# Optimization experiments

Measured on AMD Instinct MI355X. Metric: run time of the kernel, lower is better.

Reference implementation:

```python
import jax, jax.numpy as jnp
import numpy as np

B, LQ, LK, D = 32, 2048, 2048, 64


def setup_inputs() -> dict:
    key = jax.random.key(0)
    k1, k2, k3, k4 = jax.random.split(key, 4)
    querys = jax.random.normal(k1, (B, LQ, D), dtype=jnp.float32)
    keys = jax.random.normal(k2, (B, LK, D), dtype=jnp.float32)
    values = jax.random.normal(k3, (B, LK, D), dtype=jnp.float32)
    # valid lengths in [1, LK]
    valid_lens = jax.random.randint(k4, (B,), 1, LK + 1, dtype=jnp.int32)
    return {"querys": querys, "keys": keys, "values": values, "valid_lens": valid_lens}


def reference(querys, keys, values, valid_lens):
    d = querys.shape[-1]
    # [B, Lq, Lk] score matrix
    scores = jnp.einsum("bqd,bkd->bqk", querys, keys) / jnp.sqrt(jnp.asarray(d, querys.dtype))
    # masked softmax: key positions >= valid_len get -1e6 (as in d2l masked_softmax)
    key_pos = jnp.arange(scores.shape[-1], dtype=jnp.int32)  # [Lk]
    mask = key_pos[None, None, :] < valid_lens[:, None, None]  # [B, 1, Lk]
    scores = jnp.where(mask, scores, jnp.asarray(-1e6, scores.dtype))
    attn = jax.nn.softmax(scores, axis=-1)
    # dropout p=0.0 -> identity
    return jnp.einsum("bqk,bkd->bqd", attn, values)
```

## Files before the change

### kernel.cpp

```cpp
#include <hip/hip_runtime.h>
#include <hip/hip_bf16.h>
#include <math.h>


#define B_    32
#define LQ_   2048
#define LK_   2048
#define D_    64

typedef __attribute__((ext_vector_type(8)))  short bf16x8;
typedef __attribute__((ext_vector_type(4)))  float f32x4;
typedef __attribute__((ext_vector_type(16))) float f32x16;
typedef __attribute__((ext_vector_type(2)))  unsigned u32x2;

static __device__ __forceinline__ unsigned pk_bf16(float a, float b) {
    __hip_bfloat162 h = __float22bfloat162_rn(float2{a, b});
    return *(unsigned*)&h;
}

static __device__ __forceinline__ u32x2 plswap(unsigned a, unsigned b) {
    return __builtin_amdgcn_permlane32_swap(a, b, false, false);
}
static __device__ __forceinline__ float xhalf_max(float x) {
    u32x2 r = plswap(__float_as_uint(x), __float_as_uint(x));
    return fmaxf(__uint_as_float(r[0]), __uint_as_float(r[1]));
}
static __device__ __forceinline__ float xhalf_add(float x) {
    u32x2 r = plswap(__float_as_uint(x), __float_as_uint(x));
    return __uint_as_float(r[0]) + __uint_as_float(r[1]);
}

template<int NS>
__global__ __launch_bounds__(256, 6) void fa_split10_kernel(
    const float* __restrict__ Q, const float* __restrict__ K,
    const float* __restrict__ V, const int* __restrict__ vlen,
    float* __restrict__ OP, float* __restrict__ ML)
{
    __shared__ __align__(16) short Kl[2][64 * 64];
    __shared__ __align__(16) short Vt[2][64 * 64];

    const int tid  = threadIdx.x;
    const int wid  = tid >> 6;
    const int lane = tid & 63;
    const int c31  = lane & 31;
    const int h    = lane >> 5;

    constexpr int PB = 16 * NS;
    const int L    = blockIdx.x;
    const int rank = L / PB;
    const int sub  = L % PB;
    const int qb   = sub & 15;
    const int s    = sub >> 4;
    int b;
    {
        const int vj = vlen[c31];
        int r = 0;
#pragma unroll
        for (int k = 0; k < 32; ++k) {
            const int vk = __shfl(vj, k);
            r += (vk > vj) || (vk == vj && k < c31);
        }
        const unsigned long long match = __ballot(r == rank);
        b = (int)(__ffsll(match) - 1) & 31;
    }
    const int q0 = qb * 128 + wid * 32;
    const int vl = vlen[b];
    const int nt    = (vl + 63) >> 6;
    const int chunk = (nt + NS - 1) / NS;
    const int t0    = s * chunk;
    const int t1    = min(t0 + chunk, nt);

    const float qscale = 0.125f * 1.44269504088896340736f;

    unsigned qfrag[4][4];
#pragma unroll
    for (int ks = 0; ks < 4; ++ks) {
        const float* qp = Q + ((size_t)(b * LQ_ + q0 + c31)) * D_ + ks * 16 + h * 8;
        f32x4 t0v = *(const f32x4*)qp;
        f32x4 t1v = *(const f32x4*)(qp + 4);
#pragma unroll
        for (int jj = 0; jj < 2; ++jj) {
            qfrag[ks][jj]     = pk_bf16(t0v[2*jj] * qscale, t0v[2*jj+1] * qscale);
            qfrag[ks][jj + 2] = pk_bf16(t1v[2*jj] * qscale, t1v[2*jj+1] * qscale);
        }
    }

    f32x16 oacc[2];
#pragma unroll
    for (int dt = 0; dt < 2; ++dt)
#pragma unroll
        for (int r = 0; r < 16; ++r) oacc[dt][r] = 0.f;
    float mrun = -INFINITY, lrun = 0.f;

    const int skey = tid >> 2, skh = tid & 3;
    const int vkg = tid >> 4, vdg = tid & 15;

    const float* kgp = K + ((size_t)(b * LK_ + skey)) * D_ + skh * 16;
    const float* vgp = V + ((size_t)(b * LK_ + vkg * 4)) * D_ + vdg * 4;

    f32x4 kr[4], vr[4];
    if (t0 < t1) {
        const size_t off = (size_t)t0 * 64 * D_;
#pragma unroll
        for (int i = 0; i < 4; ++i) kr[i] = *(const f32x4*)(kgp + off + 4 * i);
#pragma unroll
        for (int i = 0; i < 4; ++i) vr[i] = *(const f32x4*)(vgp + off + (size_t)i * D_);
    }

    for (int t = t0; t < t1; ++t) {
        const int k0 = t * 64;
        const int buf = t & 1;

        {
            unsigned pk32[8];
#pragma unroll
            for (int m = 0; m < 8; ++m)
                pk32[m] = pk_bf16(kr[m >> 1][2 * (m & 1)], kr[m >> 1][2 * (m & 1) + 1]);
#pragma unroll
            for (int cch = 0; cch < 2; ++cch) {
                const int pos = (skh * 2 + cch) ^ (skey & 7);
                *(bf16x8*)&Kl[buf][skey * 64 + pos * 8] = *(bf16x8*)&pk32[4 * cch];
            }
#pragma unroll
            for (int dr = 0; dr < 4; ++dr) {
                const unsigned w0 = pk_bf16(vr[0][dr], vr[1][dr]);
                const unsigned w1 = pk_bf16(vr[2][dr], vr[3][dr]);
                const int dim = vdg * 4 + dr;
                const int pos = (vkg >> 1) ^ (dim & 7);
                uint2* dst = (uint2*)&Vt[buf][dim * 64 + pos * 8 + (vkg & 1) * 4];
                *dst = uint2{w0, w1};
            }
        }
        __syncthreads();

        if (t + 1 < t1) {
            const float* kn = kgp + (size_t)(k0 + 64) * D_;
            const float* vn = vgp + (size_t)(k0 + 64) * D_;
#pragma unroll
            for (int i = 0; i < 4; ++i) kr[i] = *(const f32x4*)(kn + 4 * i);
#pragma unroll
            for (int i = 0; i < 4; ++i) vr[i] = *(const f32x4*)(vn + (size_t)i * D_);
        }

        f32x16 st[2];
#pragma unroll
        for (int ss = 0; ss < 2; ++ss) {
#pragma unroll
            for (int r = 0; r < 16; ++r) st[ss][r] = 0.f;
#pragma unroll
            for (int ks = 0; ks < 4; ++ks) {
                const int pos = (ks * 2 + h) ^ (c31 & 7);
                bf16x8 kf = *(const bf16x8*)&Kl[buf][(ss * 32 + c31) * 64 + pos * 8];
                st[ss] = __builtin_amdgcn_mfma_f32_32x32x16_bf16(
                    kf, *(const bf16x8*)&qfrag[ks][0], st[ss], 0, 0, 0);
            }
        }

        if (k0 + 64 > vl) {
#pragma unroll
            for (int ss = 0; ss < 2; ++ss) {
                const int base = k0 + ss * 32 + 4 * h;
#pragma unroll
                for (int r = 0; r < 16; ++r) {
                    const int key = base + (r & 3) + 8 * (r >> 2);
                    if (key >= vl) st[ss][r] = -1e30f;
                }
            }
        }

        float m8[8];
#pragma unroll
        for (int r = 0; r < 8; ++r)
            m8[r] = fmaxf(fmaxf(st[0][r], st[0][r + 8]),
                          fmaxf(st[1][r], st[1][r + 8]));
#pragma unroll
        for (int o = 4; o; o >>= 1)
#pragma unroll
            for (int r = 0; r < o; ++r) m8[r] = fmaxf(m8[r], m8[r + o]);
        const float tm = xhalf_max(m8[0]);

        if (__any(tm > mrun + 8.f)) {
            const float mnew = fmaxf(mrun, tm);
            const float corr = exp2f(mrun - mnew);
            lrun *= corr;
#pragma unroll
            for (int dt = 0; dt < 2; ++dt)
#pragma unroll
                for (int r = 0; r < 16; ++r) oacc[dt][r] *= corr;
            mrun = mnew;
        }
#pragma unroll
        for (int ss = 0; ss < 2; ++ss)
#pragma unroll
            for (int r = 0; r < 16; ++r)
                st[ss][r] = exp2f(st[ss][r] - mrun);
        float s8[8];
#pragma unroll
        for (int r = 0; r < 8; ++r)
            s8[r] = (st[0][r] + st[0][r + 8]) + (st[1][r] + st[1][r + 8]);
#pragma unroll
        for (int o = 4; o; o >>= 1)
#pragma unroll
            for (int r = 0; r < o; ++r) s8[r] += s8[r + o];
        lrun += xhalf_add(s8[0]);

        unsigned pk[2][8];
#pragma unroll
        for (int ss = 0; ss < 2; ++ss)
#pragma unroll
            for (int m = 0; m < 8; ++m)
                pk[ss][m] = pk_bf16(st[ss][2 * m], st[ss][2 * m + 1]);

#pragma unroll
        for (int kq = 0; kq < 4; ++kq) {
            const int ss = kq >> 1, A4 = (kq & 1) * 4;
            u32x2 r02 = plswap(pk[ss][A4],     pk[ss][A4 + 2]);
            u32x2 r13 = plswap(pk[ss][A4 + 1], pk[ss][A4 + 3]);
            unsigned pf[4] = {r02[0], r13[0], r02[1], r13[1]};
            const bf16x8 pfr = *(const bf16x8*)&pf[0];
#pragma unroll
            for (int dt = 0; dt < 2; ++dt) {
                const int pos = (kq * 2 + h) ^ (c31 & 7);
                bf16x8 vf = *(const bf16x8*)&Vt[buf][(dt * 32 + c31) * 64 + pos * 8];
                oacc[dt] = __builtin_amdgcn_mfma_f32_32x32x16_bf16(vf, pfr, oacc[dt], 0, 0, 0);
            }
        }
    }

    const size_t row = (size_t)s * (B_ * LQ_) + b * LQ_ + q0 + c31;
    float* op = OP + row * D_;
#pragma unroll
    for (int dt = 0; dt < 2; ++dt)
#pragma unroll
        for (int g = 0; g < 4; ++g) {
            f32x4 v;
#pragma unroll
            for (int j = 0; j < 4; ++j) v[j] = oacc[dt][4 * g + j];
            *(f32x4*)(op + dt * 32 + 8 * g + 4 * h) = v;
        }
    if (h == 0)
        *(float2*)&ML[row * 2] = float2{mrun, lrun};
}

template<int NS>
__global__ __launch_bounds__(256) void fa_merge_kernel(
    const float* __restrict__ OP, const float* __restrict__ ML,
    float* __restrict__ O)
{
    const int g   = blockIdx.x * 256 + threadIdx.x;
    const int row = g >> 4;
    const int qd  = (g & 15) * 4;

    float mf = -INFINITY;
#pragma unroll
    for (int s = 0; s < NS; ++s) {
        float2 ml = *(const float2*)&ML[((size_t)s * (B_ * LQ_) + row) * 2];
        mf = fmaxf(mf, ml.x);
    }
    float den = 0.f;
    f32x4 acc = {0.f, 0.f, 0.f, 0.f};
#pragma unroll
    for (int s = 0; s < NS; ++s) {
        const size_t srow = (size_t)s * (B_ * LQ_) + row;
        float2 ml = *(const float2*)&ML[srow * 2];
        const float c = exp2f(ml.x - mf);
        den += c * ml.y;
        f32x4 v = *(const f32x4*)&OP[srow * D_ + qd];
        acc += v * c;
    }
    const float inv = 1.f / den;
    *(f32x4*)(O + (size_t)row * D_ + qd) = acc * inv;
}

__global__ __launch_bounds__(128, 2) void fa_mono_kernel(
    const float* __restrict__ Q, const float* __restrict__ K,
    const float* __restrict__ V, const int* __restrict__ vlen,
    float* __restrict__ O)
{
    __shared__ __align__(16) short Kl[2][64 * 64];
    __shared__ __align__(16) short Vt[2][64 * 64];

    const int tid  = threadIdx.x;
    const int wave = tid >> 6;
    const int lane = tid & 63;
    const int c31  = lane & 31;
    const int h    = lane >> 5;

    const int b  = blockIdx.y;
    const int q0 = blockIdx.x * 64 + wave * 32;
    const int vl = vlen[b];
    const int nt = (vl + 63) >> 6;

    const float qscale = 0.125f * 1.44269504088896340736f;

    unsigned qfrag[4][4];
#pragma unroll
    for (int ks = 0; ks < 4; ++ks) {
        const float* qp = Q + ((size_t)(b * LQ_ + q0 + c31)) * D_ + ks * 16 + h * 8;
        f32x4 t0 = *(const f32x4*)qp;
        f32x4 t1 = *(const f32x4*)(qp + 4);
#pragma unroll
        for (int jj = 0; jj < 2; ++jj) {
            qfrag[ks][jj]     = pk_bf16(t0[2*jj] * qscale, t0[2*jj+1] * qscale);
            qfrag[ks][jj + 2] = pk_bf16(t1[2*jj] * qscale, t1[2*jj+1] * qscale);
        }
    }

    f32x16 oacc[2];
#pragma unroll
    for (int dt = 0; dt < 2; ++dt)
#pragma unroll
        for (int r = 0; r < 16; ++r) oacc[dt][r] = 0.f;
    float mrun = -INFINITY, lrun = 0.f;

    const int skey = tid >> 1, skh = tid & 1;
    const int vkg = tid >> 4, vdg = tid & 15;

    const float* kgp = K + ((size_t)(b * LK_ + skey)) * D_ + skh * 32;
    const float* vgp = V + ((size_t)(b * LK_ + vkg * 8)) * D_ + vdg * 4;

    f32x4 kr[8], vr[8];
#pragma unroll
    for (int i = 0; i < 8; ++i) kr[i] = *(const f32x4*)(kgp + 4 * i);
#pragma unroll
    for (int i = 0; i < 8; ++i) vr[i] = *(const f32x4*)(vgp + (size_t)i * D_);

    for (int t = 0; t < nt; ++t) {
        const int k0 = t * 64;
        const int buf = t & 1;
        {
            unsigned pk32[16];
#pragma unroll
            for (int m = 0; m < 16; ++m)
                pk32[m] = pk_bf16(kr[m >> 1][2 * (m & 1)], kr[m >> 1][2 * (m & 1) + 1]);
#pragma unroll
            for (int cch = 0; cch < 4; ++cch) {
                const int pos = (skh * 4 + cch) ^ (skey & 7);
                *(bf16x8*)&Kl[buf][skey * 64 + pos * 8] = *(bf16x8*)&pk32[4 * cch];
            }
#pragma unroll
            for (int dr = 0; dr < 4; ++dr) {
                unsigned w[4];
#pragma unroll
                for (int p = 0; p < 4; ++p)
                    w[p] = pk_bf16(vr[2 * p][dr], vr[2 * p + 1][dr]);
                const int dim = vdg * 4 + dr;
                const int pos = vkg ^ (dim & 7);
                *(bf16x8*)&Vt[buf][dim * 64 + pos * 8] = *(bf16x8*)&w[0];
            }
        }
        if (t + 1 < nt) {
            const float* kn = kgp + (size_t)(k0 + 64) * D_;
            const float* vn = vgp + (size_t)(k0 + 64) * D_;
#pragma unroll
            for (int i = 0; i < 8; ++i) kr[i] = *(const f32x4*)(kn + 4 * i);
#pragma unroll
            for (int i = 0; i < 8; ++i) vr[i] = *(const f32x4*)(vn + (size_t)i * D_);
        }
        __syncthreads();

        f32x16 st[2];
#pragma unroll
        for (int ss = 0; ss < 2; ++ss) {
#pragma unroll
            for (int r = 0; r < 16; ++r) st[ss][r] = 0.f;
#pragma unroll
            for (int ks = 0; ks < 4; ++ks) {
                const int pos = (ks * 2 + h) ^ (c31 & 7);
                bf16x8 kf = *(const bf16x8*)&Kl[buf][(ss * 32 + c31) * 64 + pos * 8];
                st[ss] = __builtin_amdgcn_mfma_f32_32x32x16_bf16(
                    kf, *(const bf16x8*)&qfrag[ks][0], st[ss], 0, 0, 0);
            }
        }
        if (k0 + 64 > vl) {
#pragma unroll
            for (int ss = 0; ss < 2; ++ss) {
                const int base = k0 + ss * 32 + 4 * h;
#pragma unroll
                for (int r = 0; r < 16; ++r) {
                    const int key = base + (r & 3) + 8 * (r >> 2);
                    if (key >= vl) st[ss][r] = -1e30f;
                }
            }
        }
        float tm = st[0][0];
#pragma unroll
        for (int ss = 0; ss < 2; ++ss)
#pragma unroll
            for (int r = 0; r < 16; ++r) tm = fmaxf(tm, st[ss][r]);
        tm = fmaxf(tm, __shfl_xor(tm, 32));
        if (__any(tm > mrun + 8.f)) {
            const float mnew = fmaxf(mrun, tm);
            const float corr = exp2f(mrun - mnew);
            lrun *= corr;
#pragma unroll
            for (int dt = 0; dt < 2; ++dt)
#pragma unroll
                for (int r = 0; r < 16; ++r) oacc[dt][r] *= corr;
            mrun = mnew;
        }
        float rs = 0.f;
#pragma unroll
        for (int ss = 0; ss < 2; ++ss)
#pragma unroll
            for (int r = 0; r < 16; ++r) {
                const float p = exp2f(st[ss][r] - mrun);
                st[ss][r] = p;
                rs += p;
            }
        rs += __shfl_xor(rs, 32);
        lrun += rs;

        unsigned pk[2][8];
#pragma unroll
        for (int ss = 0; ss < 2; ++ss)
#pragma unroll
            for (int m = 0; m < 8; ++m)
                pk[ss][m] = pk_bf16(st[ss][2 * m], st[ss][2 * m + 1]);
#pragma unroll
        for (int kq = 0; kq < 4; ++kq) {
            const int ss = kq >> 1, A4 = (kq & 1) * 4;
            unsigned p0 = pk[ss][A4], p1 = pk[ss][A4+1], p2 = pk[ss][A4+2], p3 = pk[ss][A4+3];
            unsigned xp0 = __shfl_xor((int)p0, 32);
            unsigned xp1 = __shfl_xor((int)p1, 32);
            unsigned xp2 = __shfl_xor((int)p2, 32);
            unsigned xp3 = __shfl_xor((int)p3, 32);
            unsigned pf[4];
            pf[0] = h ? xp2 : p0;
            pf[1] = h ? xp3 : p1;
            pf[2] = h ? p2  : xp0;
            pf[3] = h ? p3  : xp1;
            const bf16x8 pfr = *(const bf16x8*)&pf[0];
#pragma unroll
            for (int dt = 0; dt < 2; ++dt) {
                const int pos = (kq * 2 + h) ^ (c31 & 7);
                bf16x8 vf = *(const bf16x8*)&Vt[buf][(dt * 32 + c31) * 64 + pos * 8];
                oacc[dt] = __builtin_amdgcn_mfma_f32_32x32x16_bf16(vf, pfr, oacc[dt], 0, 0, 0);
            }
        }
    }

    const float inv = 1.f / lrun;
    float* op = O + ((size_t)(b * LQ_ + q0 + c31)) * D_;
#pragma unroll
    for (int dt = 0; dt < 2; ++dt)
#pragma unroll
        for (int g = 0; g < 4; ++g) {
            f32x4 v;
#pragma unroll
            for (int j = 0; j < 4; ++j) v[j] = oacc[dt][4 * g + j] * inv;
            *(f32x4*)(op + dt * 32 + 8 * g + 4 * h) = v;
        }
}

extern "C" void kernel_launch(void* const* d_in, const int* in_sizes, int n_in,
                              void* d_out, int out_size, void* d_ws, size_t ws_size,
                              hipStream_t stream) {
    const float* Q    = (const float*)d_in[0];
    const float* K    = (const float*)d_in[1];
    const float* V    = (const float*)d_in[2];
    const int*   vlen = (const int*)d_in[3];
    float*       O    = (float*)d_out;

    const size_t rows = (size_t)B_ * LQ_;
    auto need = [&](int ns) { return (size_t)ns * rows * (D_ + 2) * sizeof(float); };

    int NS = 0;
    if      (d_ws && ws_size >= need(4)) NS = 4;
    else if (d_ws && ws_size >= need(2)) NS = 2;
    else if (d_ws && ws_size >= need(1)) NS = 1;

    if (NS == 0) {
        dim3 grid(LQ_ / 64, B_);
        fa_mono_kernel<<<grid, dim3(128), 0, stream>>>(Q, K, V, vlen, O);
        return;
    }

    float* OP = (float*)d_ws;
    float* ML = (float*)d_ws + (size_t)NS * rows * D_;

    const unsigned nblk = (unsigned)(16 * B_ * NS);
    switch (NS) {
        case 4: fa_split10_kernel<4><<<dim3(nblk), dim3(256), 0, stream>>>(Q, K, V, vlen, OP, ML); break;
        case 2: fa_split10_kernel<2><<<dim3(nblk), dim3(256), 0, stream>>>(Q, K, V, vlen, OP, ML); break;
        default: fa_split10_kernel<1><<<dim3(nblk), dim3(256), 0, stream>>>(Q, K, V, vlen, OP, ML); break;
    }

    dim3 g2((unsigned)((rows * (D_ / 4)) / 256));
    switch (NS) {
        case 4: fa_merge_kernel<4><<<g2, dim3(256), 0, stream>>>(OP, ML, O); break;
        case 2: fa_merge_kernel<2><<<g2, dim3(256), 0, stream>>>(OP, ML, O); break;
        default: fa_merge_kernel<1><<<g2, dim3(256), 0, stream>>>(OP, ML, O); break;
    }
}
```

Measured before the change: 161.4 us.

## Pre-convert K/V to bf16 (V transposed) and store split partials in bf16

```diff
diff --git a/kernel.cpp b/kernel.cpp
--- a/kernel.cpp
+++ b/kernel.cpp
@@ -17,6 +17,12 @@
     __hip_bfloat162 h = __float22bfloat162_rn(float2{a, b});
     return *(unsigned*)&h;
 }
+static __device__ __forceinline__ float bf_lo(unsigned u) {
+    return __uint_as_float(u << 16);
+}
+static __device__ __forceinline__ float bf_hi(unsigned u) {
+    return __uint_as_float(u & 0xffff0000u);
+}
 
 static __device__ __forceinline__ u32x2 plswap(unsigned a, unsigned b) {
     return __builtin_amdgcn_permlane32_swap(a, b, false, false);
@@ -30,11 +36,48 @@
     return __uint_as_float(r[0]) + __uint_as_float(r[1]);
 }
 
+__global__ __launch_bounds__(256) void fa_cvt_kernel(
+    const float* __restrict__ K, const float* __restrict__ V,
+    short* __restrict__ Kb, short* __restrict__ Vtb)
+{
+    const int tid = threadIdx.x;
+    const int b   = blockIdx.y;
+    const int k0  = blockIdx.x * 64;
+
+    {
+        const int kk = tid >> 2, q4 = tid & 3;
+        const size_t off = ((size_t)(b * LK_ + k0 + kk)) * D_ + q4 * 16;
+        const float* src = K + off;
+        unsigned w[8];
+#pragma unroll
+        for (int i = 0; i < 4; ++i) {
+            f32x4 v = *(const f32x4*)(src + 4 * i);
+            w[2 * i]     = pk_bf16(v[0], v[1]);
+            w[2 * i + 1] = pk_bf16(v[2], v[3]);
+        }
+        short* dst = Kb + off;
+        *(bf16x8*)dst       = *(bf16x8*)&w[0];
+        *(bf16x8*)(dst + 8) = *(bf16x8*)&w[4];
+    }
+    {
+        const int vkg = tid & 15, vdg = tid >> 4;
+        f32x4 vv[4];
+#pragma unroll
+        for (int p = 0; p < 4; ++p)
+            vv[p] = *(const f32x4*)&V[((size_t)(b * LK_ + k0 + vkg * 4 + p)) * D_ + vdg * 4];
+#pragma unroll
+        for (int dr = 0; dr < 4; ++dr) {
+            uint2 w = { pk_bf16(vv[0][dr], vv[1][dr]), pk_bf16(vv[2][dr], vv[3][dr]) };
+            *(uint2*)&Vtb[((size_t)(b * 64 + vdg * 4 + dr)) * LK_ + k0 + vkg * 4] = w;
+        }
+    }
+}
+
 template<int NS>
-__global__ __launch_bounds__(256, 6) void fa_split10_kernel(
-    const float* __restrict__ Q, const float* __restrict__ K,
-    const float* __restrict__ V, const int* __restrict__ vlen,
-    float* __restrict__ OP, float* __restrict__ ML)
+__global__ __launch_bounds__(256, 2) void fa_split12_kernel(
+    const float* __restrict__ Q, const short* __restrict__ Kb,
+    const short* __restrict__ Vtb, const int* __restrict__ vlen,
+    short* __restrict__ OP, float* __restrict__ ML)
 {
     __shared__ __align__(16) short Kl[2][64 * 64];
     __shared__ __align__(16) short Vt[2][64 * 64];
@@ -93,18 +136,19 @@
     float mrun = -INFINITY, lrun = 0.f;
 
     const int skey = tid >> 2, skh = tid & 3;
-    const int vkg = tid >> 4, vdg = tid & 15;
-
-    const float* kgp = K + ((size_t)(b * LK_ + skey)) * D_ + skh * 16;
-    const float* vgp = V + ((size_t)(b * LK_ + vkg * 4)) * D_ + vdg * 4;
-
-    f32x4 kr[4], vr[4];
+    const int vdim = skey, vkh = skh;
+
+    const short* kbp = Kb  + ((size_t)(b * LK_ + skey)) * D_ + skh * 16;
+    const short* vtp = Vtb + ((size_t)(b * 64 + vdim)) * LK_ + vkh * 16;
+
+    bf16x8 kr0, kr1, vr0, vr1;
     if (t0 < t1) {
-        const size_t off = (size_t)t0 * 64 * D_;
-#pragma unroll
-        for (int i = 0; i < 4; ++i) kr[i] = *(const f32x4*)(kgp + off + 4 * i);
-#pragma unroll
-        for (int i = 0; i < 4; ++i) vr[i] = *(const f32x4*)(vgp + off + (size_t)i * D_);
+        const short* kp = kbp + (size_t)t0 * 64 * D_;
+        const short* vp = vtp + (size_t)t0 * 64;
+        kr0 = *(const bf16x8*)(kp);
+        kr1 = *(const bf16x8*)(kp + 8);
+        vr0 = *(const bf16x8*)(vp);
+        vr1 = *(const bf16x8*)(vp + 8);
     }
 
     for (int t = t0; t < t1; ++t) {
@@ -112,34 +156,24 @@
         const int buf = t & 1;
 
         {
-            unsigned pk32[8];
-#pragma unroll
-            for (int m = 0; m < 8; ++m)
-                pk32[m] = pk_bf16(kr[m >> 1][2 * (m & 1)], kr[m >> 1][2 * (m & 1) + 1]);
-#pragma unroll
-            for (int cch = 0; cch < 2; ++cch) {
-                const int pos = (skh * 2 + cch) ^ (skey & 7);
-                *(bf16x8*)&Kl[buf][skey * 64 + pos * 8] = *(bf16x8*)&pk32[4 * cch];
-            }
-#pragma unroll
-            for (int dr = 0; dr < 4; ++dr) {
-                const unsigned w0 = pk_bf16(vr[0][dr], vr[1][dr]);
-                const unsigned w1 = pk_bf16(vr[2][dr], vr[3][dr]);
-                const int dim = vdg * 4 + dr;
-                const int pos = (vkg >> 1) ^ (dim & 7);
-                uint2* dst = (uint2*)&Vt[buf][dim * 64 + pos * 8 + (vkg & 1) * 4];
-                *dst = uint2{w0, w1};
-            }
+            const int pk0 = (skh * 2)     ^ (skey & 7);
+            const int pk1 = (skh * 2 + 1) ^ (skey & 7);
+            *(bf16x8*)&Kl[buf][skey * 64 + pk0 * 8] = kr0;
+            *(bf16x8*)&Kl[buf][skey * 64 + pk1 * 8] = kr1;
+            const int pv0 = (vkh * 2)     ^ (vdim & 7);
+            const int pv1 = (vkh * 2 + 1) ^ (vdim & 7);
+            *(bf16x8*)&Vt[buf][vdim * 64 + pv0 * 8] = vr0;
+            *(bf16x8*)&Vt[buf][vdim * 64 + pv1 * 8] = vr1;
         }
         __syncthreads();
 
         if (t + 1 < t1) {
-            const float* kn = kgp + (size_t)(k0 + 64) * D_;
-            const float* vn = vgp + (size_t)(k0 + 64) * D_;
-#pragma unroll
-            for (int i = 0; i < 4; ++i) kr[i] = *(const f32x4*)(kn + 4 * i);
-#pragma unroll
-            for (int i = 0; i < 4; ++i) vr[i] = *(const f32x4*)(vn + (size_t)i * D_);
+            const short* kp = kbp + (size_t)(k0 + 64) * D_;
+            const short* vp = vtp + (size_t)(k0 + 64);
+            kr0 = *(const bf16x8*)(kp);
+            kr1 = *(const bf16x8*)(kp + 8);
+            vr0 = *(const bf16x8*)(vp);
+            vr1 = *(const bf16x8*)(vp + 8);
         }
 
         f32x16 st[2];
@@ -228,15 +262,14 @@
     }
 
     const size_t row = (size_t)s * (B_ * LQ_) + b * LQ_ + q0 + c31;
-    float* op = OP + row * D_;
+    short* op = OP + row * D_;
 #pragma unroll
     for (int dt = 0; dt < 2; ++dt)
 #pragma unroll
         for (int g = 0; g < 4; ++g) {
-            f32x4 v;
-#pragma unroll
-            for (int j = 0; j < 4; ++j) v[j] = oacc[dt][4 * g + j];
-            *(f32x4*)(op + dt * 32 + 8 * g + 4 * h) = v;
+            const unsigned w0 = pk_bf16(oacc[dt][4 * g],     oacc[dt][4 * g + 1]);
+            const unsigned w1 = pk_bf16(oacc[dt][4 * g + 2], oacc[dt][4 * g + 3]);
+            *(uint2*)(op + dt * 32 + 8 * g + 4 * h) = uint2{w0, w1};
         }
     if (h == 0)
         *(float2*)&ML[row * 2] = float2{mrun, lrun};
@@ -244,7 +277,7 @@
 
 template<int NS>
 __global__ __launch_bounds__(256) void fa_merge_kernel(
-    const float* __restrict__ OP, const float* __restrict__ ML,
+    const short* __restrict__ OP, const float* __restrict__ ML,
     float* __restrict__ O)
 {
     const int g   = blockIdx.x * 256 + threadIdx.x;
@@ -265,8 +298,11 @@
         float2 ml = *(const float2*)&ML[srow * 2];
         const float c = exp2f(ml.x - mf);
         den += c * ml.y;
-        f32x4 v = *(const f32x4*)&OP[srow * D_ + qd];
-        acc += v * c;
+        uint2 w = *(const uint2*)&OP[srow * D_ + qd];
+        acc[0] += bf_lo(w.x) * c;
+        acc[1] += bf_hi(w.x) * c;
+        acc[2] += bf_lo(w.y) * c;
+        acc[3] += bf_hi(w.y) * c;
     }
     const float inv = 1.f / den;
     *(f32x4*)(O + (size_t)row * D_ + qd) = acc * inv;
@@ -462,34 +498,30 @@
     const int*   vlen = (const int*)d_in[3];
     float*       O    = (float*)d_out;
 
-    const size_t rows = (size_t)B_ * LQ_;
-    auto need = [&](int ns) { return (size_t)ns * rows * (D_ + 2) * sizeof(float); };
-
-    int NS = 0;
-    if      (d_ws && ws_size >= need(4)) NS = 4;
-    else if (d_ws && ws_size >= need(2)) NS = 2;
-    else if (d_ws && ws_size >= need(1)) NS = 1;
-
-    if (NS == 0) {
-        dim3 grid(LQ_ / 64, B_);
-        fa_mono_kernel<<<grid, dim3(128), 0, stream>>>(Q, K, V, vlen, O);
+    const size_t rows    = (size_t)B_ * LQ_;
+    const size_t kvElems = (size_t)B_ * LK_ * D_;
+    constexpr int NS = 4;
+    const size_t opBytes = (size_t)NS * rows * D_ * sizeof(short);
+    const size_t mlBytes = (size_t)NS * rows * 2 * sizeof(float);
+    const size_t kvBytes = 2 * kvElems * sizeof(short);
+    const size_t needAll = opBytes + mlBytes + kvBytes;
+
+    if (d_ws && ws_size >= needAll) {
+        short* OP  = (short*)d_ws;
+        float* ML  = (float*)((char*)d_ws + opBytes);
+        short* Kb  = (short*)((char*)d_ws + opBytes + mlBytes);
+        short* Vtb = Kb + kvElems;
+
+        fa_cvt_kernel<<<dim3(LK_ / 64, B_), dim3(256), 0, stream>>>(K, V, Kb, Vtb);
+
+        const unsigned nblk = (unsigned)(16 * B_ * NS);
+        fa_split12_kernel<NS><<<dim3(nblk), dim3(256), 0, stream>>>(Q, Kb, Vtb, vlen, OP, ML);
+
+        dim3 g2((unsigned)((rows * (D_ / 4)) / 256));
+        fa_merge_kernel<NS><<<g2, dim3(256), 0, stream>>>(OP, ML, O);
         return;
     }
 
-    float* OP = (float*)d_ws;
-    float* ML = (float*)d_ws + (size_t)NS * rows * D_;
-
-    const unsigned nblk = (unsigned)(16 * B_ * NS);
-    switch (NS) {
-        case 4: fa_split10_kernel<4><<<dim3(nblk), dim3(256), 0, stream>>>(Q, K, V, vlen, OP, ML); break;
-        case 2: fa_split10_kernel<2><<<dim3(nblk), dim3(256), 0, stream>>>(Q, K, V, vlen, OP, ML); break;
-        default: fa_split10_kernel<1><<<dim3(nblk), dim3(256), 0, stream>>>(Q, K, V, vlen, OP, ML); break;
-    }
-
-    dim3 g2((unsigned)((rows * (D_ / 4)) / 256));
-    switch (NS) {
-        case 4: fa_merge_kernel<4><<<g2, dim3(256), 0, stream>>>(OP, ML, O); break;
-        case 2: fa_merge_kernel<2><<<g2, dim3(256), 0, stream>>>(OP, ML, O); break;
-        default: fa_merge_kernel<1><<<g2, dim3(256), 0, stream>>>(OP, ML, O); break;
-    }
-}
+    dim3 grid(LQ_ / 64, B_);
+    fa_mono_kernel<<<grid, dim3(128), 0, stream>>>(Q, K, V, vlen, O);
+}
```

After: 148.7 us. 1.09x faster.
